# Performance work log

Hardware: AMD Instinct MI355X
Metric: run time of the kernel (lower is better)

Reference implementation:

```python
import jax, jax.numpy as jnp
import numpy as np

BETA = 0.25


def setup_inputs() -> dict:
    key = jax.random.key(0)
    k1, k2 = jax.random.split(key)
    x = jax.random.normal(k1, (32, 32, 32, 256), dtype=jnp.float32)
    codebook = jax.random.normal(k2, (1024, 256), dtype=jnp.float32)
    return {"x": x, "codebook": codebook}


def reference(x, codebook):
    D = codebook.shape[1]
    z_fla = x.reshape(-1, D)  # [N, D]
    # squared euclidean distances [N, K]
    dis = (jnp.sum(z_fla ** 2, axis=1, keepdims=True)
           + jnp.sum(codebook ** 2, axis=1)
           - 2.0 * jnp.matmul(z_fla, codebook.T))
    min_encoding_indices = jnp.argmin(dis, axis=1)  # [N] int
    z_q = codebook[min_encoding_indices].reshape(x.shape)
    loss = (jnp.mean((jax.lax.stop_gradient(z_q) - x) ** 2)
            + BETA * jnp.mean((z_q - jax.lax.stop_gradient(x)) ** 2))
    z_q = x + jax.lax.stop_gradient(z_q - x)  # straight-through
    # faithful to source: mean of the index values, then "perplexity" formula
    e_min = jnp.mean(min_encoding_indices.astype(jnp.float32), axis=0)
    perplexity = jnp.exp(-jnp.sum(e_min * jnp.log(e_min + 1e-10)))
    return (loss, z_q, perplexity, min_encoding_indices)
```

## Files before the change

### kernel.cpp

```cpp
#include <hip/hip_runtime.h>
#include <cmath>

#define NROWS 32768
#define DDIM  256
#define KCB   1024

constexpr float TAU = 0.25f;
constexpr int BSTR = 264;

typedef _Float16 half8 __attribute__((ext_vector_type(8)));
typedef _Float16 half4 __attribute__((ext_vector_type(4)));
typedef float floatx4 __attribute__((ext_vector_type(4)));

template<bool CVT>
__global__ __launch_bounds__(64) void prep_kernel(const float* __restrict__ cb,
                                                  float* __restrict__ cn,
                                                  _Float16* __restrict__ cbh,
                                                  double* __restrict__ sumsq,
                                                  int* __restrict__ sumidx,
                                                  unsigned* __restrict__ done) {
  const int k = blockIdx.x, lane = threadIdx.x;
  if (k == 0 && lane == 0) { *sumsq = 0.0; *sumidx = 0; *done = 0u; }
  float4 v = *(const float4*)(cb + (size_t)k * DDIM + lane * 4);
  if constexpr (CVT) {
    half4 h;
    h[0] = (_Float16)v.x; h[1] = (_Float16)v.y;
    h[2] = (_Float16)v.z; h[3] = (_Float16)v.w;
    *(half4*)&cbh[(size_t)k * DDIM + lane * 4] = h;
  }
  double s = (double)v.x * v.x + (double)v.y * v.y
           + (double)v.z * v.z + (double)v.w * v.w;
  #pragma unroll
  for (int off = 32; off; off >>= 1) s += __shfl_down(s, off);
  if (lane == 0) cn[k] = (float)s;
}

template<bool H>
__global__ __launch_bounds__(256, 2) void fused_kernel(
    const float* __restrict__ x,
    const float* __restrict__ cb,
    const _Float16* __restrict__ cbh,
    const float* __restrict__ cn,
    float* __restrict__ zq_out,
    float* __restrict__ idx_out,
    float* __restrict__ out_loss,
    float* __restrict__ out_perp,
    double* __restrict__ sumsq,
    int* __restrict__ sumidx,
    unsigned* __restrict__ done) {
  __shared__ __align__(16) _Float16 bs[2][32 * BSTR];
  __shared__ float cn_lds[KCB];
  __shared__ int   bidx[64];
  __shared__ int   bidx2[64];
  __shared__ float m2s[64];
  __shared__ float m3s[64];
  __shared__ __align__(16) float xrow[DDIM];
  __shared__ int   plist[64];
  __shared__ int   flist[64];
  __shared__ int   npair, nflag;
  __shared__ float wred[4];
  __shared__ double rv[4];
  __shared__ int    ri[4];

  const int tid = threadIdx.x;
  const int lane = tid & 63;
  const int w = tid >> 6;
  const int q = lane >> 4;
  const int tx = lane & 15;
  const int row0 = blockIdx.x * 64;

  half8 a_hi[8], a_lo[8];
  {
    const float* xp = x + (size_t)(row0 + w * 16 + tx) * DDIM + q * 8;
    #pragma unroll
    for (int s = 0; s < 8; ++s) {
      float4 v0 = *(const float4*)(xp + s * 32);
      float4 v1 = *(const float4*)(xp + s * 32 + 4);
      half8 h, l;
      _Float16 t; float sx;
      sx = -2.f * v0.x; t = (_Float16)sx; h[0] = t; l[0] = (_Float16)(sx - (float)t);
      sx = -2.f * v0.y; t = (_Float16)sx; h[1] = t; l[1] = (_Float16)(sx - (float)t);
      sx = -2.f * v0.z; t = (_Float16)sx; h[2] = t; l[2] = (_Float16)(sx - (float)t);
      sx = -2.f * v0.w; t = (_Float16)sx; h[3] = t; l[3] = (_Float16)(sx - (float)t);
      sx = -2.f * v1.x; t = (_Float16)sx; h[4] = t; l[4] = (_Float16)(sx - (float)t);
      sx = -2.f * v1.y; t = (_Float16)sx; h[5] = t; l[5] = (_Float16)(sx - (float)t);
      sx = -2.f * v1.z; t = (_Float16)sx; h[6] = t; l[6] = (_Float16)(sx - (float)t);
      sx = -2.f * v1.w; t = (_Float16)sx; h[7] = t; l[7] = (_Float16)(sx - (float)t);
      a_hi[s] = h; a_lo[s] = l;
    }
  }
  #pragma unroll
  for (int i = 0; i < 4; ++i) cn_lds[tid + 256 * i] = cn[tid + 256 * i];
  if (tid == 0) { npair = 0; nflag = 0; }

  half8 vld[4];
  float4 vldf[8];
  auto load_stage = [&](int ct) {
    #pragma unroll
    for (int i = 0; i < 4; ++i) {
      int u = tid + 256 * i;
      if constexpr (H) {
        vld[i] = *(const half8*)&cbh[(size_t)ct * 8192 + (size_t)u * 8];
      } else {
        const float* src = cb + (size_t)ct * 8192 + (size_t)u * 8;
        vldf[2 * i]     = *(const float4*)src;
        vldf[2 * i + 1] = *(const float4*)(src + 4);
      }
    }
  };
  auto write_stage = [&](int buf) {
    #pragma unroll
    for (int i = 0; i < 4; ++i) {
      int u = tid + 256 * i;
      int e = u >> 5, c = u & 31;
      if constexpr (H) {
        *(half8*)&bs[buf][e * BSTR + c * 8] = vld[i];
      } else {
        float4 v0 = vldf[2 * i], v1 = vldf[2 * i + 1];
        half8 h;
        h[0] = (_Float16)v0.x; h[1] = (_Float16)v0.y;
        h[2] = (_Float16)v0.z; h[3] = (_Float16)v0.w;
        h[4] = (_Float16)v1.x; h[5] = (_Float16)v1.y;
        h[6] = (_Float16)v1.z; h[7] = (_Float16)v1.w;
        *(half8*)&bs[buf][e * BSTR + c * 8] = h;
      }
    }
  };

  float v1[4], v2[4], v3[4];
  int i1[4], i2[4];
  #pragma unroll
  for (int r = 0; r < 4; ++r) {
    v1[r] = INFINITY; v2[r] = INFINITY; v3[r] = INFINITY; i1[r] = 0; i2[r] = 0;
  }

  load_stage(0);
  for (int st = 0; st < 32; ++st) {
    const int buf = st & 1;
    write_stage(buf);
    __syncthreads();
    if (st + 1 < 32) load_stage(st + 1);

    floatx4 ahh[2], alh[2];
    #pragma unroll
    for (int ci = 0; ci < 2; ++ci) {
      ahh[ci] = (floatx4){0.f, 0.f, 0.f, 0.f};
      alh[ci] = (floatx4){0.f, 0.f, 0.f, 0.f};
    }

    #pragma unroll
    for (int s = 0; s < 8; ++s) {
      #pragma unroll
      for (int ci = 0; ci < 2; ++ci) {
        half8 bh = *(const half8*)&bs[buf][(ci * 16 + tx) * BSTR + (s * 4 + q) * 8];
        ahh[ci] = __builtin_amdgcn_mfma_f32_16x16x32_f16(a_hi[s], bh, ahh[ci], 0, 0, 0);
        alh[ci] = __builtin_amdgcn_mfma_f32_16x16x32_f16(a_lo[s], bh, alh[ci], 0, 0, 0);
      }
    }

    #pragma unroll
    for (int ci = 0; ci < 2; ++ci) {
      int col = st * 32 + ci * 16 + tx;
      float cnv = cn_lds[col];
      #pragma unroll
      for (int r = 0; r < 4; ++r) {
        float dist = cnv + (ahh[ci][r] + alh[ci][r]);
        if (dist < v1[r]) {
          v3[r] = v2[r]; v2[r] = v1[r]; i2[r] = i1[r];
          v1[r] = dist; i1[r] = col;
        } else if (dist < v2[r]) {
          v3[r] = v2[r]; v2[r] = dist; i2[r] = col;
        } else if (dist < v3[r]) {
          v3[r] = dist;
        }
      }
    }
  }

  #pragma unroll
  for (int off = 8; off; off >>= 1) {
    #pragma unroll
    for (int r = 0; r < 4; ++r) {
      float ov1 = __shfl_down(v1[r], off, 16);
      int   oi1 = __shfl_down(i1[r], off, 16);
      float ov2 = __shfl_down(v2[r], off, 16);
      int   oi2 = __shfl_down(i2[r], off, 16);
      float ov3 = __shfl_down(v3[r], off, 16);
      bool takeo = (ov1 < v1[r]) || (ov1 == v1[r] && oi1 < i1[r]);
      float n1v = takeo ? ov1 : v1[r];
      int   n1i = takeo ? oi1 : i1[r];
      float l1 = takeo ? v1[r] : v2[r];
      int   l1i = takeo ? i1[r] : i2[r];
      float l2 = takeo ? v2[r] : v3[r];
      float r1 = takeo ? ov2 : ov1;
      int   r1i = takeo ? oi2 : oi1;
      float r2 = takeo ? ov3 : ov2;
      bool t2 = (r1 < l1) || (r1 == l1 && r1i < l1i);
      float n2v = t2 ? r1 : l1;
      int   n2i = t2 ? r1i : l1i;
      float n3v = t2 ? fminf(r2, l1) : fminf(l2, r1);
      v1[r] = n1v; i1[r] = n1i; v2[r] = n2v; i2[r] = n2i; v3[r] = n3v;
    }
  }
  if (tx == 0) {
    #pragma unroll
    for (int r = 0; r < 4; ++r) {
      int R = w * 16 + q * 4 + r;
      bidx[R]  = i1[r];
      bidx2[R] = i2[r];
      m2s[R] = v2[r] - v1[r];
      m3s[R] = v3[r] - v1[r];
    }
  }
  __syncthreads();

  if (tid < 64) {
    if (m3s[tid] < TAU) {
      int p = atomicAdd(&nflag, 1);
      flist[p] = tid;
    } else if (m2s[tid] < TAU) {
      int p = atomicAdd(&npair, 1);
      plist[p] = tid;
    }
  }
  __syncthreads();

  for (int f = 0; f < nflag; ++f) {
    int r = flist[f];
    if (tid < 64) {
      float4 v = *(const float4*)(x + (size_t)(row0 + r) * DDIM + tid * 4);
      xrow[tid * 4 + 0] = v.x; xrow[tid * 4 + 1] = v.y;
      xrow[tid * 4 + 2] = v.z; xrow[tid * 4 + 3] = v.w;
    }
    __syncthreads();
    double bd = 1e300; int bi = 0;
    #pragma unroll
    for (int j = 0; j < 4; ++j) {
      int c = tid * 4 + j;
      const float* cp = cb + (size_t)c * DDIM;
      double s0 = 0.0, s1 = 0.0, s2 = 0.0, s3 = 0.0;
      for (int d = 0; d < DDIM; d += 4) {
        float4 cv = *(const float4*)(cp + d);
        float4 xv = *(const float4*)&xrow[d];
        double d0 = (double)xv.x - (double)cv.x; s0 = fma(d0, d0, s0);
        double d1 = (double)xv.y - (double)cv.y; s1 = fma(d1, d1, s1);
        double d2 = (double)xv.z - (double)cv.z; s2 = fma(d2, d2, s2);
        double d3 = (double)xv.w - (double)cv.w; s3 = fma(d3, d3, s3);
      }
      double s = (s0 + s1) + (s2 + s3);
      if (s < bd) { bd = s; bi = c; }
    }
    #pragma unroll
    for (int off = 32; off; off >>= 1) {
      double ov = __shfl_down(bd, off);
      int oi = __shfl_down(bi, off);
      if (ov < bd || (ov == bd && oi < bi)) { bd = ov; bi = oi; }
    }
    if (lane == 0) { rv[w] = bd; ri[w] = bi; }
    __syncthreads();
    if (tid == 0) {
      double bv = rv[0]; int bix = ri[0];
      #pragma unroll
      for (int ww = 1; ww < 4; ++ww)
        if (rv[ww] < bv || (rv[ww] == bv && ri[ww] < bix)) { bv = rv[ww]; bix = ri[ww]; }
      bidx[r] = bix;
    }
    __syncthreads();
  }

  for (int f = w; f < npair; f += 4) {
    int r = plist[f];
    int cA = bidx[r], cB = bidx2[r];
    int c = (lane >= 32) ? cB : cA;
    int ld = lane & 31;
    const float* xp = x  + (size_t)(row0 + r) * DDIM + ld * 8;
    const float* cp = cb + (size_t)c * DDIM + ld * 8;
    double s = 0.0;
    #pragma unroll
    for (int j = 0; j < 8; j += 4) {
      float4 xv = *(const float4*)(xp + j);
      float4 cv = *(const float4*)(cp + j);
      double d0 = (double)xv.x - (double)cv.x; s = fma(d0, d0, s);
      double d1 = (double)xv.y - (double)cv.y; s = fma(d1, d1, s);
      double d2 = (double)xv.z - (double)cv.z; s = fma(d2, d2, s);
      double d3 = (double)xv.w - (double)cv.w; s = fma(d3, d3, s);
    }
    #pragma unroll
    for (int off = 16; off; off >>= 1) s += __shfl_xor(s, off);
    double dA = __shfl(s, 0), dB = __shfl(s, 32);
    if (lane == 0) {
      bool takeB = (dB < dA) || (dB == dA && cB < cA);
      bidx[r] = takeB ? cB : cA;
    }
  }
  __syncthreads();

  if (tid < 64) idx_out[row0 + tid] = (float)bidx[tid];

  float lsum = 0.f;
  #pragma unroll 4
  for (int it = 0; it < 16; ++it) {
    int g = tid + 256 * it;
    int r = g >> 6;
    int c4 = (g & 63) << 2;
    int k = bidx[r] & (KCB - 1);
    float4 cv = *(const float4*)(cb + (size_t)k * DDIM + c4);
    float4 xv = *(const float4*)(x + (size_t)(row0 + r) * DDIM + c4);
    float d0 = cv.x - xv.x, d1 = cv.y - xv.y, d2 = cv.z - xv.z, d3 = cv.w - xv.w;
    lsum = fmaf(d0, d0, lsum); lsum = fmaf(d1, d1, lsum);
    lsum = fmaf(d2, d2, lsum); lsum = fmaf(d3, d3, lsum);
    *(float4*)(zq_out + (size_t)(row0 + r) * DDIM + c4) = cv;
  }
  #pragma unroll
  for (int off = 32; off; off >>= 1) lsum += __shfl_down(lsum, off);
  if (lane == 0) wred[w] = lsum;
  __syncthreads();
  if (tid == 0) {
    double ls = (double)wred[0] + (double)wred[1]
              + (double)wred[2] + (double)wred[3];
    atomicAdd(sumsq, ls);
    int si = 0;
    #pragma unroll 8
    for (int r = 0; r < 64; ++r) si += bidx[r] & (KCB - 1);
    atomicAdd(sumidx, si);

    __threadfence();
    unsigned prev = atomicAdd(done, 1u);
    if (prev == gridDim.x - 1) {
      __threadfence();
      double ss = atomicAdd(sumsq, 0.0);
      int    sidx = atomicAdd(sumidx, 0);
      double loss = 1.25 * ss / 8388608.0;
      double e_min = (double)sidx / 32768.0;
      double perp = exp(-e_min * log(e_min + 1e-10));
      *out_loss = (float)loss;
      *out_perp = (float)perp;
    }
  }
}

extern "C" void kernel_launch(void* const* d_in, const int* in_sizes, int n_in,
                              void* d_out, int out_size, void* d_ws, size_t ws_size,
                              hipStream_t stream) {
  const float* x  = (const float*)d_in[0];
  const float* cb = (const float*)d_in[1];
  float* out = (float*)d_out;
  float* out_loss = out;
  float* out_zq   = out + 1;
  float* out_perp = out + 1 + 8388608;
  float* out_idx  = out + 2 + 8388608;

  double*   sumsq  = (double*)d_ws;
  int*      sumidx = (int*)((char*)d_ws + 8);
  unsigned* done   = (unsigned*)((char*)d_ws + 12);
  float*    cn     = (float*)((char*)d_ws + 64);
  _Float16* cbh    = (_Float16*)((char*)d_ws + 8192);

  const bool useH = ws_size >= (size_t)(8192 + 524288);

  if (useH) {
    hipLaunchKernelGGL(prep_kernel<true>, dim3(KCB), dim3(64), 0, stream,
                       cb, cn, cbh, sumsq, sumidx, done);
    hipLaunchKernelGGL(fused_kernel<true>, dim3(NROWS / 64), dim3(256), 0, stream,
                       x, cb, cbh, cn, out_zq, out_idx, out_loss, out_perp,
                       sumsq, sumidx, done);
  } else {
    hipLaunchKernelGGL(prep_kernel<false>, dim3(KCB), dim3(64), 0, stream,
                       cb, cn, cbh, sumsq, sumidx, done);
    hipLaunchKernelGGL(fused_kernel<false>, dim3(NROWS / 64), dim3(256), 0, stream,
                       x, cb, cbh, cn, out_zq, out_idx, out_loss, out_perp,
                       sumsq, sumidx, done);
  }
}
```

Before: 181.6 us.

## Track per-lane top-4 candidates to shrink the slow full-rescan fallback

Each lane now keeps a sorted top-4 list of candidate codes per row instead of top-3 values with two indices. After a warp reduction finds the global best, every lane adds its candidates within the tolerance band to a per-row shared list. Rows whose candidate count fits in eight get an exact double-precision recheck against the winner; only overflowing rows fall back to the full 1024-code rescan. The intent is to send fewer rows down the expensive exhaustive fallback, at the cost of more registers, shared-memory atomics and a longer insertion step in the hot loop.

```diff
diff --git a/kernel.cpp b/kernel.cpp
--- a/kernel.cpp
+++ b/kernel.cpp
@@ -51,13 +51,11 @@
   __shared__ __align__(16) _Float16 bs[2][32 * BSTR];
   __shared__ float cn_lds[KCB];
   __shared__ int   bidx[64];
-  __shared__ int   bidx2[64];
-  __shared__ float m2s[64];
-  __shared__ float m3s[64];
+  __shared__ int   clist[64][8];
+  __shared__ int   ccnt[64];
   __shared__ __align__(16) float xrow[DDIM];
-  __shared__ int   plist[64];
   __shared__ int   flist[64];
-  __shared__ int   npair, nflag;
+  __shared__ int   nflag;
   __shared__ float wred[4];
   __shared__ double rv[4];
   __shared__ int    ri[4];
@@ -91,7 +89,8 @@
   }
   #pragma unroll
   for (int i = 0; i < 4; ++i) cn_lds[tid + 256 * i] = cn[tid + 256 * i];
-  if (tid == 0) { npair = 0; nflag = 0; }
+  if (tid == 0) nflag = 0;
+  if (tid < 64) ccnt[tid] = 0;
 
   half8 vld[4];
   float4 vldf[8];
@@ -127,12 +126,12 @@
     }
   };
 
-  float v1[4], v2[4], v3[4];
-  int i1[4], i2[4];
-  #pragma unroll
-  for (int r = 0; r < 4; ++r) {
-    v1[r] = INFINITY; v2[r] = INFINITY; v3[r] = INFINITY; i1[r] = 0; i2[r] = 0;
-  }
+  float tv[4][4];
+  int   ti[4][4];
+  #pragma unroll
+  for (int r = 0; r < 4; ++r)
+    #pragma unroll
+    for (int j = 0; j < 4; ++j) { tv[r][j] = INFINITY; ti[r][j] = 0; }
 
   load_stage(0);
   for (int st = 0; st < 32; ++st) {
@@ -165,63 +164,56 @@
       #pragma unroll
       for (int r = 0; r < 4; ++r) {
         float dist = cnv + (ahh[ci][r] + alh[ci][r]);
-        if (dist < v1[r]) {
-          v3[r] = v2[r]; v2[r] = v1[r]; i2[r] = i1[r];
-          v1[r] = dist; i1[r] = col;
-        } else if (dist < v2[r]) {
-          v3[r] = v2[r]; v2[r] = dist; i2[r] = col;
-        } else if (dist < v3[r]) {
-          v3[r] = dist;
+        if (dist < tv[r][3]) {
+          if (dist < tv[r][0]) {
+            tv[r][3] = tv[r][2]; ti[r][3] = ti[r][2];
+            tv[r][2] = tv[r][1]; ti[r][2] = ti[r][1];
+            tv[r][1] = tv[r][0]; ti[r][1] = ti[r][0];
+            tv[r][0] = dist; ti[r][0] = col;
+          } else if (dist < tv[r][1]) {
+            tv[r][3] = tv[r][2]; ti[r][3] = ti[r][2];
+            tv[r][2] = tv[r][1]; ti[r][2] = ti[r][1];
+            tv[r][1] = dist; ti[r][1] = col;
+          } else if (dist < tv[r][2]) {
+            tv[r][3] = tv[r][2]; ti[r][3] = ti[r][2];
+            tv[r][2] = dist; ti[r][2] = col;
+          } else {
+            tv[r][3] = dist; ti[r][3] = col;
+          }
         }
       }
     }
   }
 
   #pragma unroll
-  for (int off = 8; off; off >>= 1) {
-    #pragma unroll
-    for (int r = 0; r < 4; ++r) {
-      float ov1 = __shfl_down(v1[r], off, 16);
-      int   oi1 = __shfl_down(i1[r], off, 16);
-      float ov2 = __shfl_down(v2[r], off, 16);
-      int   oi2 = __shfl_down(i2[r], off, 16);
-      float ov3 = __shfl_down(v3[r], off, 16);
-      bool takeo = (ov1 < v1[r]) || (ov1 == v1[r] && oi1 < i1[r]);
-      float n1v = takeo ? ov1 : v1[r];
-      int   n1i = takeo ? oi1 : i1[r];
-      float l1 = takeo ? v1[r] : v2[r];
-      int   l1i = takeo ? i1[r] : i2[r];
-      float l2 = takeo ? v2[r] : v3[r];
-      float r1 = takeo ? ov2 : ov1;
-      int   r1i = takeo ? oi2 : oi1;
-      float r2 = takeo ? ov3 : ov2;
-      bool t2 = (r1 < l1) || (r1 == l1 && r1i < l1i);
-      float n2v = t2 ? r1 : l1;
-      int   n2i = t2 ? r1i : l1i;
-      float n3v = t2 ? fminf(r2, l1) : fminf(l2, r1);
-      v1[r] = n1v; i1[r] = n1i; v2[r] = n2v; i2[r] = n2i; v3[r] = n3v;
-    }
-  }
-  if (tx == 0) {
-    #pragma unroll
-    for (int r = 0; r < 4; ++r) {
-      int R = w * 16 + q * 4 + r;
-      bidx[R]  = i1[r];
-      bidx2[R] = i2[r];
-      m2s[R] = v2[r] - v1[r];
-      m3s[R] = v3[r] - v1[r];
-    }
+  for (int r = 0; r < 4; ++r) {
+    float bv = tv[r][0]; int bi = ti[r][0];
+    #pragma unroll
+    for (int off = 8; off; off >>= 1) {
+      float ov = __shfl_down(bv, off, 16);
+      int   oi = __shfl_down(bi, off, 16);
+      if (ov < bv || (ov == bv && oi < bi)) { bv = ov; bi = oi; }
+    }
+    bv = __shfl(bv, 0, 16);
+    bi = __shfl(bi, 0, 16);
+    int R = w * 16 + q * 4 + r;
+    if (tx == 0) bidx[R] = bi;
+    float thresh = bv + TAU;
+    #pragma unroll
+    for (int j = 0; j < 4; ++j) {
+      if (tv[r][j] < thresh && !(tv[r][j] == bv && ti[r][j] == bi)) {
+        int p = atomicAdd(&ccnt[R], 1);
+        if (p < 8) clist[R][p] = ti[r][j];
+      }
+    }
+    if (tv[r][3] < thresh)
+      atomicAdd(&ccnt[R], 64);
   }
   __syncthreads();
 
-  if (tid < 64) {
-    if (m3s[tid] < TAU) {
-      int p = atomicAdd(&nflag, 1);
-      flist[p] = tid;
-    } else if (m2s[tid] < TAU) {
-      int p = atomicAdd(&npair, 1);
-      plist[p] = tid;
-    }
+  if (tid < 64 && ccnt[tid] > 7) {
+    int p = atomicAdd(&nflag, 1);
+    flist[p] = tid;
   }
   __syncthreads();
 
@@ -268,30 +260,32 @@
     __syncthreads();
   }
 
-  for (int f = w; f < npair; f += 4) {
-    int r = plist[f];
-    int cA = bidx[r], cB = bidx2[r];
-    int c = (lane >= 32) ? cB : cA;
-    int ld = lane & 31;
-    const float* xp = x  + (size_t)(row0 + r) * DDIM + ld * 8;
-    const float* cp = cb + (size_t)c * DDIM + ld * 8;
-    double s = 0.0;
-    #pragma unroll
-    for (int j = 0; j < 8; j += 4) {
-      float4 xv = *(const float4*)(xp + j);
-      float4 cv = *(const float4*)(cp + j);
-      double d0 = (double)xv.x - (double)cv.x; s = fma(d0, d0, s);
-      double d1 = (double)xv.y - (double)cv.y; s = fma(d1, d1, s);
-      double d2 = (double)xv.z - (double)cv.z; s = fma(d2, d2, s);
-      double d3 = (double)xv.w - (double)cv.w; s = fma(d3, d3, s);
-    }
-    #pragma unroll
-    for (int off = 16; off; off >>= 1) s += __shfl_xor(s, off);
-    double dA = __shfl(s, 0), dB = __shfl(s, 32);
-    if (lane == 0) {
-      bool takeB = (dB < dA) || (dB == dA && cB < cA);
-      bidx[r] = takeB ? cB : cA;
-    }
+  for (int r = w; r < 64; r += 4) {
+    int c = ccnt[r];
+    if (c == 0 || c > 7) continue;
+    int winner = bidx[r];
+    for (int t = 0; t < c; ++t) {
+      int cB = clist[r][t];
+      int ccol = (lane >= 32) ? cB : winner;
+      int ld = lane & 31;
+      const float* xp = x  + (size_t)(row0 + r) * DDIM + ld * 8;
+      const float* cp = cb + (size_t)ccol * DDIM + ld * 8;
+      double s = 0.0;
+      #pragma unroll
+      for (int j = 0; j < 8; j += 4) {
+        float4 xv = *(const float4*)(xp + j);
+        float4 cv = *(const float4*)(cp + j);
+        double d0 = (double)xv.x - (double)cv.x; s = fma(d0, d0, s);
+        double d1 = (double)xv.y - (double)cv.y; s = fma(d1, d1, s);
+        double d2 = (double)xv.z - (double)cv.z; s = fma(d2, d2, s);
+        double d3 = (double)xv.w - (double)cv.w; s = fma(d3, d3, s);
+      }
+      #pragma unroll
+      for (int off = 16; off; off >>= 1) s += __shfl_xor(s, off);
+      double dA = __shfl(s, 0), dB = __shfl(s, 32);
+      if (dB < dA || (dB == dA && cB < winner)) winner = cB;
+    }
+    if (lane == 0) bidx[r] = winner;
   }
   __syncthreads();
 
```

Measured after the change: 160.8 us. 11.4% less time.
